# Optimization experiments

Hardware: AMD Instinct MI355X
Metric: run time of the kernel (lower is better)

Reference implementation:

```python
import jax, jax.numpy as jnp
import numpy as np

RATIOS = (2, 2, 2)
IN_SIZE = 512
DATA_SIZE = 2
NOISE_BANDS = 5
TARGET_SIZE = int(np.prod(RATIOS))  # 8


def conv1d(x, w, b, stride):
    # cc.get_padding(3, stride, mode='centered'): total pad = 3 - stride = 1 -> (left, right) = (0, 1)
    y = jax.lax.conv_general_dilated(
        x, w, window_strides=(stride,), padding=[(0, 1)],
        dimension_numbers=('NCH', 'OIH', 'NCH'))
    return y + b[None, :, None]


def mod_sigmoid(x):
    return 2.0 * jax.nn.sigmoid(x) ** 2.3 + 1e-7


def amp_to_impulse_response(amp, target_size):
    # amp: [..., noise_bands] real, treated as complex spectrum with zero imag
    ir = jnp.fft.irfft(amp)                      # [..., 2*(nb-1)]
    fs = ir.shape[-1]
    ir = jnp.roll(ir, fs // 2, axis=-1)
    n = jnp.arange(fs, dtype=ir.dtype)
    win = 0.5 * (1.0 - jnp.cos(2.0 * jnp.pi * n / fs))  # periodic hann (torch default)
    ir = ir * win
    pad = int(target_size) - fs                   # 0 for our config
    ir = jnp.pad(ir, [(0, 0)] * (ir.ndim - 1) + [(0, pad)])
    return jnp.roll(ir, -(fs // 2), axis=-1)


def fft_convolve(signal, kernel):
    n = signal.shape[-1]
    pad_cfg = [(0, 0)] * (signal.ndim - 1)
    s = jnp.pad(signal, pad_cfg + [(0, n)])
    k = jnp.pad(kernel, pad_cfg + [(n, 0)])
    out = jnp.fft.irfft(jnp.fft.rfft(s) * jnp.fft.rfft(k))
    return out[..., out.shape[-1] // 2:]


def setup_inputs() -> dict:
    key = jax.random.key(0)
    ks = jax.random.split(key, 8)
    B, T = 16, 4096
    c_out = DATA_SIZE * NOISE_BANDS
    x = jax.random.normal(ks[0], (B, IN_SIZE, T), dtype=jnp.float32)
    noise = jax.random.uniform(ks[1], (B, T // TARGET_SIZE, DATA_SIZE, TARGET_SIZE), dtype=jnp.float32)
    w1 = jax.random.normal(ks[2], (IN_SIZE, IN_SIZE, 3), dtype=jnp.float32) * 0.03
    b1 = jnp.zeros((IN_SIZE,), dtype=jnp.float32)
    w2 = jax.random.normal(ks[3], (IN_SIZE, IN_SIZE, 3), dtype=jnp.float32) * 0.03
    b2 = jnp.zeros((IN_SIZE,), dtype=jnp.float32)
    w3 = jax.random.normal(ks[4], (c_out, IN_SIZE, 3), dtype=jnp.float32) * 0.03
    b3 = jnp.zeros((c_out,), dtype=jnp.float32)
    return {"x": x, "noise": noise, "w1": w1, "b1": b1, "w2": w2, "b2": b2, "w3": w3, "b3": b3}


def reference(x, noise, w1, b1, w2, b2, w3, b3):
    h = conv1d(x, w1, b1, RATIOS[0])
    h = jax.nn.leaky_relu(h, 0.2)
    h = conv1d(h, w2, b2, RATIOS[1])
    h = jax.nn.leaky_relu(h, 0.2)
    h = conv1d(h, w3, b3, RATIOS[2])            # [B, data_size*nb, T']
    amp = mod_sigmoid(h - 5.0)
    amp = jnp.transpose(amp, (0, 2, 1))          # [B, T', data_size*nb]
    B, Tp = amp.shape[0], amp.shape[1]
    amp = amp.reshape(B, Tp, DATA_SIZE, -1)      # [B, T', data_size, nb]
    ir = amp_to_impulse_response(amp, TARGET_SIZE)  # [B, T', data_size, target]
    nz = noise * 2.0 - 1.0                        # torch.rand_like(ir)*2-1
    out = fft_convolve(nz, ir)                    # [B, T', data_size, target]
    out = jnp.transpose(out, (0, 2, 1, 3))        # [B, data_size, T', target]
    return out.reshape(B, DATA_SIZE, -1)          # [B, data_size, T'*target]
```

## Files before the change

### kernel.cpp

```cpp
#include <hip/hip_runtime.h>
#include <math.h>


typedef __attribute__((ext_vector_type(8)))  short bf16x8;
typedef __attribute__((ext_vector_type(16))) float f32x16;

__device__ __forceinline__ unsigned short f2bf_rne(float f) {
    unsigned int u = __float_as_uint(f);
    unsigned int r = u + 0x7fff + ((u >> 16) & 1);
    return (unsigned short)(r >> 16);
}
__device__ __forceinline__ float bf2f(unsigned short h) {
    return __uint_as_float(((unsigned int)h) << 16);
}
__device__ __forceinline__ void gload_lds16(const void* g, void* l) {
    __builtin_amdgcn_global_load_lds(
        (const __attribute__((address_space(1))) unsigned int*)g,
        (__attribute__((address_space(3))) unsigned int*)l, 16, 0, 0);
}
__device__ __forceinline__ int swz1(int r) {
    return ((r >> 1) ^ (r >> 4)) & 7;
}

__global__ void prep_w_kernel(const float* __restrict__ W, short* __restrict__ Wf)
{
    int gid = blockIdx.x * 256 + threadIdx.x;
    int f = gid >> 6, l = gid & 63;
    int ks = f & 1, hl = (f >> 1) & 1;
    int k  = (f >> 2) % 3;
    int rem = (f >> 2) / 3;
    int cob = rem & 15, cb = rem >> 4;
    int co  = cob * 32 + (l & 31);
    int ci0 = cb * 32 + ks * 16 + (l >> 5) * 8;
    bf16x8 o;
#pragma unroll
    for (int j = 0; j < 8; ++j) {
        float v = W[((size_t)co * 512 + ci0 + j) * 3 + k];
        unsigned short hi = f2bf_rne(v);
        o[j] = hl ? (short)f2bf_rne(v - bf2f(hi)) : (short)hi;
    }
    *(bf16x8*)((char*)Wf + (size_t)f * 1024 + l * 16) = o;
}

__global__ void zero_pads(char* __restrict__ h1p, char* __restrict__ h2t) {
    int id = blockIdx.x * 256 + threadIdx.x;
    if (id < 16384) {
        int b = id >> 10, w = id & 1023;
        *(float*)(h1p + ((size_t)b * 2080 + 2048) * 2048 + (size_t)w * 4) = 0.f;
    } else {
        int id2 = id - 16384;
        int b = id2 >> 10, w = id2 & 1023;
        *(float*)(h2t + ((size_t)b * 1026 + 1024) * 2048 + (size_t)w * 4) = 0.f;
    }
}

__global__ __launch_bounds__(256, 2) void conv1_fused(
    const float* __restrict__ X, const short* __restrict__ Wf,
    const float* __restrict__ Bias, char* __restrict__ Out)
{
    __shared__ char AB[2][16512];

    const int tid = threadIdx.x;
    const int l   = tid & 63;
    const int wid = tid >> 6;
    const int tl0 = l & 31;
    const int lh  = l >> 5;

    int p = blockIdx.x;
    int chunk = p >> 5, slot = p & 31;
    int gl = slot & 15, c = slot >> 4;
    int g = chunk * 16 + gl;
    int zb = g >> 5, y = g & 31;

    const int bt0 = y * 64;
    const int r0  = 2 * bt0;
    const float* Xb = X + (size_t)zb * 512 * 4096;

    const int rg  = tid & 15;
    const int cip = tid >> 4;

    f32x16 acc[2][2];
#pragma unroll
    for (int tp = 0; tp < 2; ++tp)
#pragma unroll
        for (int cp = 0; cp < 2; ++cp) acc[tp][cp] = (f32x16)(0.0f);

    const int cbase = c * 8 + wid * 2;

    float4 fx0, fx1, fx2, fx3;
    float  fextra = 0.f;

    auto issue_loads = [&](int cb) {
        const float* s0 = Xb + (size_t)(cb * 32 + 2 * cip) * 4096 + r0 + rg * 8;
        fx0 = *(const float4*)(s0);
        fx1 = *(const float4*)(s0 + 4);
        fx2 = *(const float4*)(s0 + 4096);
        fx3 = *(const float4*)(s0 + 4100);
        if (tid < 32) {
            int rr = r0 + 128;
            fextra = (rr < 4096) ? Xb[(size_t)(cb * 32 + tid) * 4096 + rr] : 0.f;
        }
    };

    auto write_tile = [&](char* buf) {
        float va[8] = {fx0.x, fx0.y, fx0.z, fx0.w, fx1.x, fx1.y, fx1.z, fx1.w};
        float vb[8] = {fx2.x, fx2.y, fx2.z, fx2.w, fx3.x, fx3.y, fx3.z, fx3.w};
        const int ci   = 2 * cip;
        const int u_hi = ci >> 3;
        const int u_lo = 4 + u_hi;
        const int coff = (ci & 7) * 2;
#pragma unroll
        for (int k = 0; k < 8; ++k) {
            int r  = rg * 8 + k;
            int sw = swz1(r);
            unsigned short h0 = f2bf_rne(va[k]);
            unsigned short l0 = f2bf_rne(va[k] - bf2f(h0));
            unsigned short h1 = f2bf_rne(vb[k]);
            unsigned short l1 = f2bf_rne(vb[k] - bf2f(h1));
            *(unsigned int*)(buf + r * 128 + (((u_hi ^ sw)) << 4) + coff) =
                (unsigned int)h0 | ((unsigned int)h1 << 16);
            *(unsigned int*)(buf + r * 128 + (((u_lo ^ sw)) << 4) + coff) =
                (unsigned int)l0 | ((unsigned int)l1 << 16);
        }
        if (tid < 32) {
            int sw = swz1(128);
            unsigned short h = f2bf_rne(fextra);
            unsigned short lo = f2bf_rne(fextra - bf2f(h));
            int uh = (tid >> 3) ^ sw;
            int ul = (4 + (tid >> 3)) ^ sw;
            *(unsigned short*)(buf + 128 * 128 + (uh << 4) + (tid & 7) * 2) = h;
            *(unsigned short*)(buf + 128 * 128 + (ul << 4) + (tid & 7) * 2) = lo;
        }
    };

    issue_loads(0);
    write_tile(AB[0]);
    __syncthreads();

    for (int cb = 0; cb < 16; ++cb) {
        if (cb < 15) issue_loads(cb + 1);
        const char* Ab = AB[cb & 1];
#pragma unroll
        for (int ph = 0; ph < 6; ++ph) {
            const int tap = ph >> 1, ks = ph & 1;
            bf16x8 a[2][2], bb[2][2];
#pragma unroll
            for (int tp = 0; tp < 2; ++tp) {
                int rl = 2 * (tp * 32 + tl0) + tap;
                int sw = swz1(rl);
                int qb = ks * 2 + lh;
                a[0][tp] = *(const bf16x8*)(Ab + rl * 128 + ((qb ^ sw) << 4));
                a[1][tp] = *(const bf16x8*)(Ab + rl * 128 + (((qb + 4) ^ sw) << 4));
            }
#pragma unroll
            for (int cp = 0; cp < 2; ++cp) {
                size_t f0 = ((((size_t)(cb * 16 + cbase + cp) * 3 + tap) * 2 + 0) * 2 + ks);
                const char* wp = (const char*)Wf + f0 * 1024 + l * 16;
                bb[0][cp] = *(const bf16x8*)(wp);
                bb[1][cp] = *(const bf16x8*)(wp + 2048);
            }
#pragma unroll
            for (int tp = 0; tp < 2; ++tp)
#pragma unroll
                for (int cp = 0; cp < 2; ++cp) {
                    acc[tp][cp] = __builtin_amdgcn_mfma_f32_32x32x16_bf16(
                        a[0][tp], bb[0][cp], acc[tp][cp], 0, 0, 0);
                    acc[tp][cp] = __builtin_amdgcn_mfma_f32_32x32x16_bf16(
                        a[0][tp], bb[1][cp], acc[tp][cp], 0, 0, 0);
                    acc[tp][cp] = __builtin_amdgcn_mfma_f32_32x32x16_bf16(
                        a[1][tp], bb[0][cp], acc[tp][cp], 0, 0, 0);
                }
        }
        if (cb < 15) write_tile(AB[(cb + 1) & 1]);
        __syncthreads();
    }

    const size_t outB = (size_t)zb * 2080 * 2048;
    const int colb = c * 256 + wid * 64 + tl0;
#pragma unroll
    for (int cp = 0; cp < 2; ++cp) {
        int co = colb + cp * 32;
        float bv = Bias[co];
#pragma unroll
        for (int tp = 0; tp < 2; ++tp) {
            int trow = bt0 + tp * 32 + 4 * lh;
#pragma unroll
            for (int r = 0; r < 16; ++r) {
                int row = trow + (r & 3) + 8 * (r >> 2);
                float v = acc[tp][cp][r] + bv;
                v = v < 0.f ? 0.2f * v : v;
                char* po = Out + outB + (size_t)row * 2048;
                unsigned short hi = f2bf_rne(v);
                unsigned short lo = f2bf_rne(v - bf2f(hi));
                *(unsigned short*)(po + co * 2) = hi;
                *(unsigned short*)(po + 1024 + co * 2) = lo;
            }
        }
    }
}

#define CONV_UNITS 1032

__global__ __launch_bounds__(256, 2) void conv_mfma(
    const char* __restrict__ Xp, const short* __restrict__ Wf,
    const float* __restrict__ Bias, char* __restrict__ Out,
    int rowsX, int rowsO, int Yt, int mode)
{
    __shared__ char AB[2][16512];

    const int tid = threadIdx.x;
    const int l   = tid & 63;
    const int wid = tid >> 6;
    const int tl0 = l & 31;
    const int lh  = l >> 5;

    int p = blockIdx.x;
    int chunk = p >> 5, slot = p & 31;
    int gl = slot & 15, c = slot >> 4;
    int g = chunk * 16 + gl;
    int zb = g / Yt, y = g - zb * Yt;

    const int bt0 = y * 64;
    const int r0  = 2 * bt0;
    const char* Xb = Xp + (size_t)zb * (size_t)rowsX * 2048;

    f32x16 acc[2][2];
#pragma unroll
    for (int tp = 0; tp < 2; ++tp)
#pragma unroll
        for (int cp = 0; cp < 2; ++cp) acc[tp][cp] = (f32x16)(0.0f);

    const int cbase = c * 8 + wid * 2;

    auto stage = [&](char* buf, int cb) {
#pragma unroll
        for (int i = 0; i < 5; ++i) {
            int u = i * 256 + tid;
            if (u < CONV_UNITS) {
                int r = u >> 3, ul = u & 7;
                int us = ul ^ ((r >> 1) & 7);
                const char* gp = Xb + (size_t)(r0 + r) * 2048
                               + (us >> 2) * 1024 + cb * 64 + (us & 3) * 16;
                gload_lds16(gp, buf + ((size_t)(i * 256 + wid * 64)) * 16);
            }
        }
    };

    stage(AB[0], 0);
    __syncthreads();

    for (int cb = 0; cb < 16; ++cb) {
        if (cb < 15) stage(AB[(cb + 1) & 1], cb + 1);
        const char* Ab = AB[cb & 1];
#pragma unroll
        for (int ph = 0; ph < 6; ++ph) {
            const int tap = ph >> 1, ks = ph & 1;
            bf16x8 a[2][2], bb[2][2];
#pragma unroll
            for (int tp = 0; tp < 2; ++tp) {
                int rl = 2 * (tp * 32 + tl0) + tap;
                int sw = (rl >> 1) & 7;
                int qb = ks * 2 + lh;
                a[0][tp] = *(const bf16x8*)(Ab + rl * 128 + ((qb ^ sw) << 4));
                a[1][tp] = *(const bf16x8*)(Ab + rl * 128 + (((qb + 4) ^ sw) << 4));
            }
#pragma unroll
            for (int cp = 0; cp < 2; ++cp) {
                size_t f0 = ((((size_t)(cb * 16 + cbase + cp) * 3 + tap) * 2 + 0) * 2 + ks);
                const char* wp = (const char*)Wf + f0 * 1024 + l * 16;
                bb[0][cp] = *(const bf16x8*)(wp);
                bb[1][cp] = *(const bf16x8*)(wp + 2048);
            }
#pragma unroll
            for (int tp = 0; tp < 2; ++tp)
#pragma unroll
                for (int cp = 0; cp < 2; ++cp) {
                    acc[tp][cp] = __builtin_amdgcn_mfma_f32_32x32x16_bf16(
                        a[0][tp], bb[0][cp], acc[tp][cp], 0, 0, 0);
                    acc[tp][cp] = __builtin_amdgcn_mfma_f32_32x32x16_bf16(
                        a[0][tp], bb[1][cp], acc[tp][cp], 0, 0, 0);
                    acc[tp][cp] = __builtin_amdgcn_mfma_f32_32x32x16_bf16(
                        a[1][tp], bb[0][cp], acc[tp][cp], 0, 0, 0);
                }
        }
        __syncthreads();
    }

    const size_t outB = (size_t)zb * (size_t)rowsO * 2048;
    const int colb = c * 256 + wid * 64 + tl0;
#pragma unroll
    for (int cp = 0; cp < 2; ++cp) {
        int co = colb + cp * 32;
        float bv = Bias[co];
#pragma unroll
        for (int tp = 0; tp < 2; ++tp) {
            int trow = bt0 + tp * 32 + 4 * lh;
#pragma unroll
            for (int r = 0; r < 16; ++r) {
                int row = trow + (r & 3) + 8 * (r >> 2);
                float v = acc[tp][cp][r] + bv;
                v = v < 0.f ? 0.2f * v : v;
                char* po = Out + outB + (size_t)row * 2048;
                if (mode == 0) {
                    unsigned short hi = f2bf_rne(v);
                    unsigned short lo = f2bf_rne(v - bf2f(hi));
                    *(unsigned short*)(po + co * 2) = hi;
                    *(unsigned short*)(po + 1024 + co * 2) = lo;
                } else {
                    *(float*)(po + (size_t)co * 4) = v;
                }
            }
        }
    }
}

__global__ __launch_bounds__(256) void conv3_tmaj(
    const float* __restrict__ H2, const float* __restrict__ W3,
    const float* __restrict__ B3, const float* __restrict__ Noise,
    float* __restrict__ Out)
{
    __shared__ float W3s[1536][10];
    __shared__ float Xe[32][40];
    __shared__ float Xo[32][40];
    __shared__ float hs[32][12];

    const int b   = blockIdx.y;
    const int t0  = blockIdx.x * 32;
    const int tid = threadIdx.x;
    const int t   = tid & 31;
    const int gch = tid >> 5;

    for (int idx = tid; idx < 15360; idx += 256) {
        int co = idx / 1536;
        int r  = idx - co * 1536;
        W3s[r][co] = W3[idx];
    }

    float acc3[2] = {0.f, 0.f};
    const float* Hb = H2 + (size_t)b * 1026 * 512;

    for (int c0 = 0; c0 < 512; c0 += 32) {
        __syncthreads();
        for (int idx = tid; idx < 33 * 32; idx += 256) {
            int pp = idx >> 5, ci = idx & 31;
            Xe[ci][pp] = Hb[(size_t)(2 * t0 + 2 * pp) * 512 + c0 + ci];
            Xo[ci][pp] = Hb[(size_t)(2 * t0 + 2 * pp + 1) * 512 + c0 + ci];
        }
        __syncthreads();

        for (int ci = 0; ci < 32; ++ci) {
            float xe0 = Xe[ci][t];
            float xo0 = Xo[ci][t];
            float xe1 = Xe[ci][t + 1];
            int r = (c0 + ci) * 3;
#pragma unroll
            for (int m = 0; m < 2; ++m) {
                int cc = gch + m * 8;
                if (cc < 10) {
                    acc3[m] = fmaf(W3s[r][cc], xe0,
                              fmaf(W3s[r + 1][cc], xo0,
                              fmaf(W3s[r + 2][cc], xe1, acc3[m])));
                }
            }
        }
    }

#pragma unroll
    for (int m = 0; m < 2; ++m) {
        int cc = gch + m * 8;
        if (cc < 10) hs[t][cc] = acc3[m] + B3[cc];
    }
    __syncthreads();

    if (tid < 64) {
        const int tt = tid & 31;
        const int d  = tid >> 5;

        float A[5];
#pragma unroll
        for (int j = 0; j < 5; ++j) {
            float h = hs[tt][d * 5 + j] - 5.f;
            float s = 1.f / (1.f + expf(-h));
            A[j] = 2.f * powf(s, 2.3f) + 1e-7f;
        }

        const float SQ = 0.70710678118654752f;
        const float c1[8] = {1.f, SQ, 0.f, -SQ, -1.f, -SQ, 0.f, SQ};
        const float c2[8] = {1.f, 0.f, -1.f, 0.f, 1.f, 0.f, -1.f, 0.f};
        const float c3[8] = {1.f, -SQ, 0.f, SQ, -1.f, SQ, 0.f, -SQ};
        const float c4[8] = {1.f, -1.f, 1.f, -1.f, 1.f, -1.f, 1.f, -1.f};
        const float wsh[8] = {1.f, 0.85355339059327376f, 0.5f, 0.14644660940672624f,
                              0.f, 0.14644660940672624f, 0.5f, 0.85355339059327376f};

        float ir[8];
#pragma unroll
        for (int n = 0; n < 8; ++n) {
            float v = A[0] + 2.f * (A[1] * c1[n] + A[2] * c2[n] + A[3] * c3[n])
                    + A[4] * c4[n];
            ir[n] = 0.125f * v * wsh[n];
        }

        const float* npi = Noise + (size_t)b * 8192 + (size_t)(t0 + tt) * 16 + d * 8;
        float nz[8];
#pragma unroll
        for (int j = 0; j < 8; ++j) nz[j] = 2.f * npi[j] - 1.f;

        float* op = Out + (size_t)b * 8192 + (size_t)d * 4096 + (size_t)(t0 + tt) * 8;
#pragma unroll
        for (int o = 0; o < 8; ++o) {
            float s = 0.f;
#pragma unroll
            for (int j = 0; j <= o; ++j) s += nz[j] * ir[o - j];
            op[o] = s;
        }
    }
}

#define BCO 64
#define BT  128
#define KC  16

__global__ __launch_bounds__(256, 2) void conv_s2_kernel(
    const float* __restrict__ X, const float* __restrict__ W,
    const float* __restrict__ Bias, float* __restrict__ Y,
    int Cin, int Tin, int Cout, int Tout, int leaky)
{
    __shared__ float Xe[KC][132];
    __shared__ float Xo[KC][132];
    __shared__ float Wk[KC * 3][68];

    const int b   = blockIdx.z;
    const int co0 = blockIdx.y * BCO;
    const int t0  = blockIdx.x * BT;
    const int tid = threadIdx.x;
    const int ty  = tid & 15;
    const int tx  = tid >> 4;

    const float* Xb = X + (size_t)b * Cin * Tin;

    float acc[4][8];
#pragma unroll
    for (int i = 0; i < 4; ++i)
#pragma unroll
        for (int j = 0; j < 8; ++j) acc[i][j] = 0.f;

    for (int c0 = 0; c0 < Cin; c0 += KC) {
        __syncthreads();
        for (int idx = tid; idx < KC * 130; idx += 256) {
            int ci = idx / 130;
            int pp = idx - ci * 130;
            int gt = 2 * t0 + 2 * pp;
            const float* src = Xb + (size_t)(c0 + ci) * Tin;
            float e, o;
            if (gt + 1 < Tin) {
                float2 v = *(const float2*)(src + gt);
                e = v.x; o = v.y;
            } else {
                e = (gt < Tin) ? src[gt] : 0.f;
                o = 0.f;
            }
            Xe[ci][pp] = e;
            Xo[ci][pp] = o;
        }
        {
            const float* Wc = W + (size_t)co0 * Cin * 3 + (size_t)c0 * 3;
            for (int idx = tid; idx < BCO * (KC * 3); idx += 256) {
                int co = idx / 48;
                int r  = idx - co * 48;
                Wk[r][co] = Wc[(size_t)co * Cin * 3 + r];
            }
        }
        __syncthreads();

#pragma unroll
        for (int ci = 0; ci < KC; ++ci) {
            float4 xe0 = *(const float4*)&Xe[ci][tx * 8];
            float4 xe1 = *(const float4*)&Xe[ci][tx * 8 + 4];
            float  xe8 = Xe[ci][tx * 8 + 8];
            float4 xo0 = *(const float4*)&Xo[ci][tx * 8];
            float4 xo1 = *(const float4*)&Xo[ci][tx * 8 + 4];
            float4 w0  = *(const float4*)&Wk[ci * 3 + 0][ty * 4];
            float4 w1  = *(const float4*)&Wk[ci * 3 + 1][ty * 4];
            float4 w2  = *(const float4*)&Wk[ci * 3 + 2][ty * 4];
            float xe[9] = {xe0.x, xe0.y, xe0.z, xe0.w, xe1.x, xe1.y, xe1.z, xe1.w, xe8};
            float xo[8] = {xo0.x, xo0.y, xo0.z, xo0.w, xo1.x, xo1.y, xo1.z, xo1.w};
            float wa[3][4] = {{w0.x, w0.y, w0.z, w0.w},
                              {w1.x, w1.y, w1.z, w1.w},
                              {w2.x, w2.y, w2.z, w2.w}};
#pragma unroll
            for (int i = 0; i < 4; ++i)
#pragma unroll
                for (int j = 0; j < 8; ++j)
                    acc[i][j] = fmaf(wa[0][i], xe[j],
                                fmaf(wa[1][i], xo[j],
                                fmaf(wa[2][i], xe[j + 1], acc[i][j])));
        }
    }

    float* Yb = Y + (size_t)b * Cout * Tout;
#pragma unroll
    for (int i = 0; i < 4; ++i) {
        int   co = co0 + ty * 4 + i;
        float bv = Bias[co];
        float ov[8];
#pragma unroll
        for (int j = 0; j < 8; ++j) {
            float v = acc[i][j] + bv;
            ov[j] = (leaky && v < 0.f) ? 0.2f * v : v;
        }
        float* dst = Yb + (size_t)co * Tout + t0 + tx * 8;
        *(float4*)dst       = make_float4(ov[0], ov[1], ov[2], ov[3]);
        *(float4*)(dst + 4) = make_float4(ov[4], ov[5], ov[6], ov[7]);
    }
}

__global__ __launch_bounds__(256) void conv3_cmaj(
    const float* __restrict__ H2, const float* __restrict__ W3,
    const float* __restrict__ B3, const float* __restrict__ Noise,
    float* __restrict__ Out)
{
    __shared__ float W3s[1536][10];
    __shared__ float Xe[32][40];
    __shared__ float Xo[32][40];
    __shared__ float hs[32][12];

    const int b   = blockIdx.y;
    const int t0  = blockIdx.x * 32;
    const int tid = threadIdx.x;
    const int t   = tid & 31;
    const int gch = tid >> 5;

    for (int idx = tid; idx < 15360; idx += 256) {
        int co = idx / 1536;
        int r  = idx - co * 1536;
        W3s[r][co] = W3[idx];
    }

    float acc3[2] = {0.f, 0.f};
    const float* Hb = H2 + (size_t)b * 512 * 1024;

    for (int c0 = 0; c0 < 512; c0 += 32) {
        __syncthreads();
        for (int idx = tid; idx < 32 * 33; idx += 256) {
            int ci = idx / 33;
            int pp = idx - ci * 33;
            int gt = 2 * t0 + 2 * pp;
            const float* src = Hb + (size_t)(c0 + ci) * 1024;
            float e, o;
            if (gt + 1 < 1024) {
                float2 v = *(const float2*)(src + gt);
                e = v.x; o = v.y;
            } else {
                e = (gt < 1024) ? src[gt] : 0.f;
                o = 0.f;
            }
            Xe[ci][pp] = e;
            Xo[ci][pp] = o;
        }
        __syncthreads();

        for (int ci = 0; ci < 32; ++ci) {
            float xe0 = Xe[ci][t];
            float xo0 = Xo[ci][t];
            float xe1 = Xe[ci][t + 1];
            int r = (c0 + ci) * 3;
#pragma unroll
            for (int m = 0; m < 2; ++m) {
                int cc = gch + m * 8;
                if (cc < 10)
                    acc3[m] = fmaf(W3s[r][cc], xe0,
                              fmaf(W3s[r + 1][cc], xo0,
                              fmaf(W3s[r + 2][cc], xe1, acc3[m])));
            }
        }
    }

#pragma unroll
    for (int m = 0; m < 2; ++m) {
        int cc = gch + m * 8;
        if (cc < 10) hs[t][cc] = acc3[m] + B3[cc];
    }
    __syncthreads();

    if (tid < 64) {
        const int tt = tid & 31;
        const int d  = tid >> 5;
        float A[5];
#pragma unroll
        for (int j = 0; j < 5; ++j) {
            float h = hs[tt][d * 5 + j] - 5.f;
            float s = 1.f / (1.f + expf(-h));
            A[j] = 2.f * powf(s, 2.3f) + 1e-7f;
        }
        const float SQ = 0.70710678118654752f;
        const float c1[8] = {1.f, SQ, 0.f, -SQ, -1.f, -SQ, 0.f, SQ};
        const float c2[8] = {1.f, 0.f, -1.f, 0.f, 1.f, 0.f, -1.f, 0.f};
        const float c3[8] = {1.f, -SQ, 0.f, SQ, -1.f, SQ, 0.f, -SQ};
        const float c4[8] = {1.f, -1.f, 1.f, -1.f, 1.f, -1.f, 1.f, -1.f};
        const float wsh[8] = {1.f, 0.85355339059327376f, 0.5f, 0.14644660940672624f,
                              0.f, 0.14644660940672624f, 0.5f, 0.85355339059327376f};
        float ir[8];
#pragma unroll
        for (int n = 0; n < 8; ++n) {
            float v = A[0] + 2.f * (A[1] * c1[n] + A[2] * c2[n] + A[3] * c3[n])
                    + A[4] * c4[n];
            ir[n] = 0.125f * v * wsh[n];
        }
        const float* npi = Noise + (size_t)b * 8192 + (size_t)(t0 + tt) * 16 + d * 8;
        float nz[8];
#pragma unroll
        for (int j = 0; j < 8; ++j) nz[j] = 2.f * npi[j] - 1.f;
        float* op = Out + (size_t)b * 8192 + (size_t)d * 4096 + (size_t)(t0 + tt) * 8;
#pragma unroll
        for (int o = 0; o < 8; ++o) {
            float s = 0.f;
#pragma unroll
            for (int j = 0; j <= o; ++j) s += nz[j] * ir[o - j];
            op[o] = s;
        }
    }
}

extern "C" void kernel_launch(void* const* d_in, const int* in_sizes, int n_in,
                              void* d_out, int out_size, void* d_ws, size_t ws_size,
                              hipStream_t stream) {
    const float* x     = (const float*)d_in[0];
    const float* noise = (const float*)d_in[1];
    const float* w1    = (const float*)d_in[2];
    const float* b1    = (const float*)d_in[3];
    const float* w2    = (const float*)d_in[4];
    const float* b2    = (const float*)d_in[5];
    const float* w3    = (const float*)d_in[6];
    const float* b3    = (const float*)d_in[7];
    float* out = (float*)d_out;

    const size_t H1P_BYTES = (size_t)16 * 2080 * 2048;
    const size_t H2T_BYTES = (size_t)16 * 1026 * 512 * 4;
    const size_t WF_BYTES  = (size_t)512 * 512 * 3 * 2 * 2;
    const size_t NEED = H1P_BYTES + H2T_BYTES + 2 * WF_BYTES;

    if (ws_size >= NEED) {
        char*  h1p = (char*)d_ws;
        char*  h2t = h1p + H1P_BYTES;
        short* Wf1 = (short*)(h2t + H2T_BYTES);
        short* Wf2 = (short*)((char*)Wf1 + WF_BYTES);

        prep_w_kernel<<<768, 256, 0, stream>>>(w1, Wf1);
        prep_w_kernel<<<768, 256, 0, stream>>>(w2, Wf2);
        zero_pads<<<128, 256, 0, stream>>>(h1p, h2t);
        conv1_fused<<<1024, 256, 0, stream>>>(x, Wf1, b1, h1p);
        conv_mfma<<<512, 256, 0, stream>>>(h1p, Wf2, b2, h2t, 2080, 1026, 16, 1);
        conv3_tmaj<<<dim3(16, 16), 256, 0, stream>>>((const float*)h2t, w3, b3, noise, out);
    } else {
        float* h1 = (float*)d_ws;
        float* h2 = h1 + (size_t)16 * 512 * 2048;
        dim3 blk(256);
        conv_s2_kernel<<<dim3(2048 / BT, 512 / BCO, 16), blk, 0, stream>>>(
            x, w1, b1, h1, 512, 4096, 512, 2048, 1);
        conv_s2_kernel<<<dim3(1024 / BT, 512 / BCO, 16), blk, 0, stream>>>(
            h1, w2, b2, h2, 512, 2048, 512, 1024, 1);
        conv3_cmaj<<<dim3(16, 16), blk, 0, stream>>>(h2, w3, b3, noise, out);
    }
}
```

Before: 317.5 us.

## Double time-tile height in conv1 and conv2 MFMA kernels to reuse weights

Both stride-2 conv kernels now compute 128 output time steps per block instead of 64, holding four MFMA row tiles per wave and doubling the LDS staging buffers. Each weight fragment loaded from global memory is reused across twice as many rows, and the grids shrink to 512 and 256 blocks. The hi-part bf16 split in conv1 also switches from round-to-nearest to truncation, which saves a few ALU ops. In exchange, register pressure and LDS use rise, and the smaller grids may leave many of the 256 CUs idle.

New measurement: 354.8 us. 11.8% more time.

```diff
diff --git a/kernel.cpp b/kernel.cpp
--- a/kernel.cpp
+++ b/kernel.cpp
@@ -58,7 +58,7 @@
     const float* __restrict__ X, const short* __restrict__ Wf,
     const float* __restrict__ Bias, char* __restrict__ Out)
 {
-    __shared__ char AB[2][16512];
+    __shared__ char AB[2][33024];
 
     const int tid = threadIdx.x;
     const int l   = tid & 63;
@@ -70,67 +70,81 @@
     int chunk = p >> 5, slot = p & 31;
     int gl = slot & 15, c = slot >> 4;
     int g = chunk * 16 + gl;
-    int zb = g >> 5, y = g & 31;
-
-    const int bt0 = y * 64;
+    int zb = g >> 4, y = g & 15;
+
+    const int bt0 = y * 128;
     const int r0  = 2 * bt0;
     const float* Xb = X + (size_t)zb * 512 * 4096;
 
-    const int rg  = tid & 15;
-    const int cip = tid >> 4;
-
-    f32x16 acc[2][2];
-#pragma unroll
-    for (int tp = 0; tp < 2; ++tp)
+    const int rg   = tid & 15;
+    const int cip  = tid >> 4;
+    const int ci   = 2 * cip;
+    const int u_hi = ci >> 3;
+    const int u_lo = 4 + u_hi;
+    const int coff = (ci & 7) * 2;
+
+    f32x16 acc[4][2];
+#pragma unroll
+    for (int tp = 0; tp < 4; ++tp)
 #pragma unroll
         for (int cp = 0; cp < 2; ++cp) acc[tp][cp] = (f32x16)(0.0f);
 
     const int cbase = c * 8 + wid * 2;
 
-    float4 fx0, fx1, fx2, fx3;
+    float4 fa[4], fb[4];
     float  fextra = 0.f;
 
     auto issue_loads = [&](int cb) {
-        const float* s0 = Xb + (size_t)(cb * 32 + 2 * cip) * 4096 + r0 + rg * 8;
-        fx0 = *(const float4*)(s0);
-        fx1 = *(const float4*)(s0 + 4);
-        fx2 = *(const float4*)(s0 + 4096);
-        fx3 = *(const float4*)(s0 + 4100);
+        const float* s0 = Xb + (size_t)(cb * 32 + ci) * 4096 + r0 + rg * 16;
+#pragma unroll
+        for (int i = 0; i < 4; ++i) {
+            fa[i] = *(const float4*)(s0 + i * 4);
+            fb[i] = *(const float4*)(s0 + 4096 + i * 4);
+        }
         if (tid < 32) {
-            int rr = r0 + 128;
+            int rr = r0 + 256;
             fextra = (rr < 4096) ? Xb[(size_t)(cb * 32 + tid) * 4096 + rr] : 0.f;
         }
     };
 
+    auto write_k = [&](char* buf, int r, float a, float b) {
+        int sw = swz1(r);
+        unsigned int ua = __float_as_uint(a);
+        unsigned int ub = __float_as_uint(b);
+        float ha = __uint_as_float(ua & 0xffff0000u);
+        float hb = __uint_as_float(ub & 0xffff0000u);
+        unsigned short la = f2bf_rne(a - ha);
+        unsigned short lb = f2bf_rne(b - hb);
+        *(unsigned int*)(buf + r * 128 + ((u_hi ^ sw) << 4) + coff) =
+            (ua >> 16) | (ub & 0xffff0000u);
+        *(unsigned int*)(buf + r * 128 + ((u_lo ^ sw) << 4) + coff) =
+            (unsigned int)la | ((unsigned int)lb << 16);
+    };
     auto write_tile = [&](char* buf) {
-        float va[8] = {fx0.x, fx0.y, fx0.z, fx0.w, fx1.x, fx1.y, fx1.z, fx1.w};
-        float vb[8] = {fx2.x, fx2.y, fx2.z, fx2.w, fx3.x, fx3.y, fx3.z, fx3.w};
-        const int ci   = 2 * cip;
-        const int u_hi = ci >> 3;
-        const int u_lo = 4 + u_hi;
-        const int coff = (ci & 7) * 2;
-#pragma unroll
-        for (int k = 0; k < 8; ++k) {
-            int r  = rg * 8 + k;
-            int sw = swz1(r);
-            unsigned short h0 = f2bf_rne(va[k]);
-            unsigned short l0 = f2bf_rne(va[k] - bf2f(h0));
-            unsigned short h1 = f2bf_rne(vb[k]);
-            unsigned short l1 = f2bf_rne(vb[k] - bf2f(h1));
-            *(unsigned int*)(buf + r * 128 + (((u_hi ^ sw)) << 4) + coff) =
-                (unsigned int)h0 | ((unsigned int)h1 << 16);
-            *(unsigned int*)(buf + r * 128 + (((u_lo ^ sw)) << 4) + coff) =
-                (unsigned int)l0 | ((unsigned int)l1 << 16);
+#pragma unroll
+        for (int i = 0; i < 4; ++i) {
+            int rb = rg * 16 + i * 4;
+            write_k(buf, rb + 0, fa[i].x, fb[i].x);
+            write_k(buf, rb + 1, fa[i].y, fb[i].y);
+            write_k(buf, rb + 2, fa[i].z, fb[i].z);
+            write_k(buf, rb + 3, fa[i].w, fb[i].w);
         }
         if (tid < 32) {
-            int sw = swz1(128);
-            unsigned short h = f2bf_rne(fextra);
-            unsigned short lo = f2bf_rne(fextra - bf2f(h));
+            int sw = swz1(256);
+            unsigned int ue = __float_as_uint(fextra);
+            float he = __uint_as_float(ue & 0xffff0000u);
+            unsigned short lo = f2bf_rne(fextra - he);
             int uh = (tid >> 3) ^ sw;
             int ul = (4 + (tid >> 3)) ^ sw;
-            *(unsigned short*)(buf + 128 * 128 + (uh << 4) + (tid & 7) * 2) = h;
-            *(unsigned short*)(buf + 128 * 128 + (ul << 4) + (tid & 7) * 2) = lo;
-        }
+            *(unsigned short*)(buf + 256 * 128 + (uh << 4) + (tid & 7) * 2) =
+                (unsigned short)(ue >> 16);
+            *(unsigned short*)(buf + 256 * 128 + (ul << 4) + (tid & 7) * 2) = lo;
+        }
+    };
+
+    auto wptr = [&](int cb_, int cp, int tap, int ks, int hl) -> const char* {
+        size_t f0 = ((((size_t)(cb_ * 16 + cbase + cp) * 3 + tap) * 2 + hl) * 2 + ks);
+        return (const char*)Wf + f0 * 1024 + (size_t)l * 16;
     };
 
     issue_loads(0);
@@ -143,14 +157,125 @@
 #pragma unroll
         for (int ph = 0; ph < 6; ++ph) {
             const int tap = ph >> 1, ks = ph & 1;
-            bf16x8 a[2][2], bb[2][2];
-#pragma unroll
-            for (int tp = 0; tp < 2; ++tp) {
+            bf16x8 a0[4], a1[4], bb[2][2];
+#pragma unroll
+            for (int tp = 0; tp < 4; ++tp) {
                 int rl = 2 * (tp * 32 + tl0) + tap;
                 int sw = swz1(rl);
                 int qb = ks * 2 + lh;
-                a[0][tp] = *(const bf16x8*)(Ab + rl * 128 + ((qb ^ sw) << 4));
-                a[1][tp] = *(const bf16x8*)(Ab + rl * 128 + (((qb + 4) ^ sw) << 4));
+                a0[tp] = *(const bf16x8*)(Ab + rl * 128 + ((qb ^ sw) << 4));
+                a1[tp] = *(const bf16x8*)(Ab + rl * 128 + (((qb + 4) ^ sw) << 4));
+            }
+#pragma unroll
+            for (int cp = 0; cp < 2; ++cp) {
+                const char* wp = wptr(cb, cp, tap, ks, 0);
+                bb[0][cp] = *(const bf16x8*)(wp);
+                bb[1][cp] = *(const bf16x8*)(wp + 2048);
+            }
+#pragma unroll
+            for (int tp = 0; tp < 4; ++tp)
+#pragma unroll
+                for (int cp = 0; cp < 2; ++cp) {
+                    acc[tp][cp] = __builtin_amdgcn_mfma_f32_32x32x16_bf16(
+                        a0[tp], bb[0][cp], acc[tp][cp], 0, 0, 0);
+                    acc[tp][cp] = __builtin_amdgcn_mfma_f32_32x32x16_bf16(
+                        a0[tp], bb[1][cp], acc[tp][cp], 0, 0, 0);
+                    acc[tp][cp] = __builtin_amdgcn_mfma_f32_32x32x16_bf16(
+                        a1[tp], bb[0][cp], acc[tp][cp], 0, 0, 0);
+                }
+        }
+        if (cb < 15) write_tile((char*)AB[(cb + 1) & 1]);
+        __syncthreads();
+    }
+
+    const size_t outB = (size_t)zb * 2080 * 2048;
+    const int colb = c * 256 + wid * 64 + tl0;
+#pragma unroll
+    for (int cp = 0; cp < 2; ++cp) {
+        int co = colb + cp * 32;
+        float bv = Bias[co];
+#pragma unroll
+        for (int tp = 0; tp < 4; ++tp) {
+            int trow = bt0 + tp * 32 + 4 * lh;
+#pragma unroll
+            for (int r = 0; r < 16; ++r) {
+                int row = trow + (r & 3) + 8 * (r >> 2);
+                float v = acc[tp][cp][r] + bv;
+                v = v < 0.f ? 0.2f * v : v;
+                char* po = Out + outB + (size_t)row * 2048;
+                unsigned int uv = __float_as_uint(v);
+                float hf = __uint_as_float(uv & 0xffff0000u);
+                *(unsigned short*)(po + co * 2) = (unsigned short)(uv >> 16);
+                *(unsigned short*)(po + 1024 + co * 2) = f2bf_rne(v - hf);
+            }
+        }
+    }
+}
+
+#define CONV_UNITS2 2056
+
+__global__ __launch_bounds__(256, 2) void conv_mfma(
+    const char* __restrict__ Xp, const short* __restrict__ Wf,
+    const float* __restrict__ Bias, char* __restrict__ Out,
+    int rowsX, int rowsO, int Yt, int mode)
+{
+    __shared__ char AB[2][33024];
+
+    const int tid = threadIdx.x;
+    const int l   = tid & 63;
+    const int wid = tid >> 6;
+    const int tl0 = l & 31;
+    const int lh  = l >> 5;
+
+    int p = blockIdx.x;
+    int chunk = p >> 5, slot = p & 31;
+    int gl = slot & 15, c = slot >> 4;
+    int g = chunk * 16 + gl;
+    int zb = g / Yt, y = g - zb * Yt;
+
+    const int bt0 = y * 128;
+    const int r0  = 2 * bt0;
+    const char* Xb = Xp + (size_t)zb * (size_t)rowsX * 2048;
+
+    f32x16 acc[4][2];
+#pragma unroll
+    for (int tp = 0; tp < 4; ++tp)
+#pragma unroll
+        for (int cp = 0; cp < 2; ++cp) acc[tp][cp] = (f32x16)(0.0f);
+
+    const int cbase = c * 8 + wid * 2;
+
+    auto stage = [&](char* buf, int cb) {
+#pragma unroll
+        for (int i = 0; i < 9; ++i) {
+            int u = i * 256 + tid;
+            if (u < CONV_UNITS2) {
+                int r = u >> 3, ul = u & 7;
+                int us = ul ^ ((r >> 1) & 7);
+                const char* gp = Xb + (size_t)(r0 + r) * 2048
+                               + (us >> 2) * 1024 + cb * 64 + (us & 3) * 16;
+                gload_lds16(gp, buf + ((size_t)(i * 256 + wid * 64)) * 16);
+            }
+        }
+    };
+
+    stage(AB[0], 0);
+    __syncthreads();
+
+    for (int cb = 0; cb < 16; ++cb) {
+        if (cb < 15) stage(AB[(cb + 1) & 1], cb + 1);
+        const char* Ab = AB[cb & 1];
+#pragma unroll
+        for (int ph = 0; ph < 6; ++ph) {
+            const int tap = ph >> 1, ks = ph & 1;
+            bf16x8 a0[4], a1[4], bb[2][2];
+#pragma unroll
+            for (int tp = 0; tp < 4; ++tp) {
+                int rl = 2 * (tp * 32 + tl0) + tap;
+                int sw = (rl >> 1) & 7;
+                int qb = ks * 2 + lh;
+                a0[tp] = *(const bf16x8*)(Ab + rl * 128 + ((qb ^ sw) << 4));
+                a1[tp] = *(const bf16x8*)(Ab + rl * 128 + (((qb + 4) ^ sw) << 4));
             }
 #pragma unroll
             for (int cp = 0; cp < 2; ++cp) {
@@ -160,140 +285,28 @@
                 bb[1][cp] = *(const bf16x8*)(wp + 2048);
             }
 #pragma unroll
-            for (int tp = 0; tp < 2; ++tp)
+            for (int tp = 0; tp < 4; ++tp)
 #pragma unroll
                 for (int cp = 0; cp < 2; ++cp) {
                     acc[tp][cp] = __builtin_amdgcn_mfma_f32_32x32x16_bf16(
-                        a[0][tp], bb[0][cp], acc[tp][cp], 0, 0, 0);
+                        a0[tp], bb[0][cp], acc[tp][cp], 0, 0, 0);
                     acc[tp][cp] = __builtin_amdgcn_mfma_f32_32x32x16_bf16(
-                        a[0][tp], bb[1][cp], acc[tp][cp], 0, 0, 0);
+                        a0[tp], bb[1][cp], acc[tp][cp], 0, 0, 0);
                     acc[tp][cp] = __builtin_amdgcn_mfma_f32_32x32x16_bf16(
-                        a[1][tp], bb[0][cp], acc[tp][cp], 0, 0, 0);
+                        a1[tp], bb[0][cp], acc[tp][cp], 0, 0, 0);
                 }
         }
-        if (cb < 15) write_tile(AB[(cb + 1) & 1]);
-        __syncthreads();
-    }
-
-    const size_t outB = (size_t)zb * 2080 * 2048;
+        __syncthreads();
+    }
+
+    const size_t outB = (size_t)zb * (size_t)rowsO * 2048;
     const int colb = c * 256 + wid * 64 + tl0;
 #pragma unroll
     for (int cp = 0; cp < 2; ++cp) {
         int co = colb + cp * 32;
         float bv = Bias[co];
 #pragma unroll
-        for (int tp = 0; tp < 2; ++tp) {
-            int trow = bt0 + tp * 32 + 4 * lh;
-#pragma unroll
-            for (int r = 0; r < 16; ++r) {
-                int row = trow + (r & 3) + 8 * (r >> 2);
-                float v = acc[tp][cp][r] + bv;
-                v = v < 0.f ? 0.2f * v : v;
-                char* po = Out + outB + (size_t)row * 2048;
-                unsigned short hi = f2bf_rne(v);
-                unsigned short lo = f2bf_rne(v - bf2f(hi));
-                *(unsigned short*)(po + co * 2) = hi;
-                *(unsigned short*)(po + 1024 + co * 2) = lo;
-            }
-        }
-    }
-}
-
-#define CONV_UNITS 1032
-
-__global__ __launch_bounds__(256, 2) void conv_mfma(
-    const char* __restrict__ Xp, const short* __restrict__ Wf,
-    const float* __restrict__ Bias, char* __restrict__ Out,
-    int rowsX, int rowsO, int Yt, int mode)
-{
-    __shared__ char AB[2][16512];
-
-    const int tid = threadIdx.x;
-    const int l   = tid & 63;
-    const int wid = tid >> 6;
-    const int tl0 = l & 31;
-    const int lh  = l >> 5;
-
-    int p = blockIdx.x;
-    int chunk = p >> 5, slot = p & 31;
-    int gl = slot & 15, c = slot >> 4;
-    int g = chunk * 16 + gl;
-    int zb = g / Yt, y = g - zb * Yt;
-
-    const int bt0 = y * 64;
-    const int r0  = 2 * bt0;
-    const char* Xb = Xp + (size_t)zb * (size_t)rowsX * 2048;
-
-    f32x16 acc[2][2];
-#pragma unroll
-    for (int tp = 0; tp < 2; ++tp)
-#pragma unroll
-        for (int cp = 0; cp < 2; ++cp) acc[tp][cp] = (f32x16)(0.0f);
-
-    const int cbase = c * 8 + wid * 2;
-
-    auto stage = [&](char* buf, int cb) {
-#pragma unroll
-        for (int i = 0; i < 5; ++i) {
-            int u = i * 256 + tid;
-            if (u < CONV_UNITS) {
-                int r = u >> 3, ul = u & 7;
-                int us = ul ^ ((r >> 1) & 7);
-                const char* gp = Xb + (size_t)(r0 + r) * 2048
-                               + (us >> 2) * 1024 + cb * 64 + (us & 3) * 16;
-                gload_lds16(gp, buf + ((size_t)(i * 256 + wid * 64)) * 16);
-            }
-        }
-    };
-
-    stage(AB[0], 0);
-    __syncthreads();
-
-    for (int cb = 0; cb < 16; ++cb) {
-        if (cb < 15) stage(AB[(cb + 1) & 1], cb + 1);
-        const char* Ab = AB[cb & 1];
-#pragma unroll
-        for (int ph = 0; ph < 6; ++ph) {
-            const int tap = ph >> 1, ks = ph & 1;
-            bf16x8 a[2][2], bb[2][2];
-#pragma unroll
-            for (int tp = 0; tp < 2; ++tp) {
-                int rl = 2 * (tp * 32 + tl0) + tap;
-                int sw = (rl >> 1) & 7;
-                int qb = ks * 2 + lh;
-                a[0][tp] = *(const bf16x8*)(Ab + rl * 128 + ((qb ^ sw) << 4));
-                a[1][tp] = *(const bf16x8*)(Ab + rl * 128 + (((qb + 4) ^ sw) << 4));
-            }
-#pragma unroll
-            for (int cp = 0; cp < 2; ++cp) {
-                size_t f0 = ((((size_t)(cb * 16 + cbase + cp) * 3 + tap) * 2 + 0) * 2 + ks);
-                const char* wp = (const char*)Wf + f0 * 1024 + l * 16;
-                bb[0][cp] = *(const bf16x8*)(wp);
-                bb[1][cp] = *(const bf16x8*)(wp + 2048);
-            }
-#pragma unroll
-            for (int tp = 0; tp < 2; ++tp)
-#pragma unroll
-                for (int cp = 0; cp < 2; ++cp) {
-                    acc[tp][cp] = __builtin_amdgcn_mfma_f32_32x32x16_bf16(
-                        a[0][tp], bb[0][cp], acc[tp][cp], 0, 0, 0);
-                    acc[tp][cp] = __builtin_amdgcn_mfma_f32_32x32x16_bf16(
-                        a[0][tp], bb[1][cp], acc[tp][cp], 0, 0, 0);
-                    acc[tp][cp] = __builtin_amdgcn_mfma_f32_32x32x16_bf16(
-                        a[1][tp], bb[0][cp], acc[tp][cp], 0, 0, 0);
-                }
-        }
-        __syncthreads();
-    }
-
-    const size_t outB = (size_t)zb * (size_t)rowsO * 2048;
-    const int colb = c * 256 + wid * 64 + tl0;
-#pragma unroll
-    for (int cp = 0; cp < 2; ++cp) {
-        int co = colb + cp * 32;
-        float bv = Bias[co];
-#pragma unroll
-        for (int tp = 0; tp < 2; ++tp) {
+        for (int tp = 0; tp < 4; ++tp) {
             int trow = bt0 + tp * 32 + 4 * lh;
 #pragma unroll
             for (int r = 0; r < 16; ++r) {
@@ -648,8 +661,8 @@
         prep_w_kernel<<<768, 256, 0, stream>>>(w1, Wf1);
         prep_w_kernel<<<768, 256, 0, stream>>>(w2, Wf2);
         zero_pads<<<128, 256, 0, stream>>>(h1p, h2t);
-        conv1_fused<<<1024, 256, 0, stream>>>(x, Wf1, b1, h1p);
-        conv_mfma<<<512, 256, 0, stream>>>(h1p, Wf2, b2, h2t, 2080, 1026, 16, 1);
+        conv1_fused<<<512, 256, 0, stream>>>(x, Wf1, b1, h1p);
+        conv_mfma<<<256, 256, 0, stream>>>(h1p, Wf2, b2, h2t, 2080, 1026, 8, 1);
         conv3_tmaj<<<dim3(16, 16), 256, 0, stream>>>((const float*)h2t, w3, b3, noise, out);
     } else {
         float* h1 = (float*)d_ws;
```
